# Kernel tuning notes

Hardware: AMD Instinct MI355X
Metric: run time of the kernel (lower is better)

## Reference

```python
import jax, jax.numpy as jnp
import numpy as np

N_HEADS = 16
N_KV_HEADS = 8
SOFTMAX_N = 1.0


def _apply_rope(t, cos, sin):
    # t: [B, S, H, HD]; cos/sin: [S, HD//2]
    tr = t[..., 0::2]
    ti = t[..., 1::2]
    c = cos[None, :, None, :]
    s = sin[None, :, None, :]
    out_r = tr * c - ti * s
    out_i = tr * s + ti * c
    # interleave back: (..., HD//2, 2) -> (..., HD)
    return jnp.stack([out_r, out_i], axis=-1).reshape(t.shape)


def setup_inputs() -> dict:
    key = jax.random.key(0)
    ks = jax.random.split(key, 7)
    B, S, D = 2, 2048, 2048
    HD = D // N_HEADS  # 128
    kv_dim = N_KV_HEADS * HD  # 1024
    # realistic RoPE frequencies
    theta = 10000.0
    inv_freq = 1.0 / (theta ** (np.arange(0, HD, 2, dtype=np.float32) / HD))
    angles = np.outer(np.arange(S, dtype=np.float32), inv_freq)  # [S, HD//2]
    scale = 0.02
    return {
        "x": jax.random.normal(ks[0], (B, S, D), dtype=jnp.float32),
        "freqs_cos": jnp.asarray(np.cos(angles), dtype=jnp.float32),
        "freqs_sin": jnp.asarray(np.sin(angles), dtype=jnp.float32),
        "wq": jax.random.normal(ks[1], (D, D), dtype=jnp.float32) * scale,
        "wk": jax.random.normal(ks[2], (D, kv_dim), dtype=jnp.float32) * scale,
        "wv": jax.random.normal(ks[3], (D, kv_dim), dtype=jnp.float32) * scale,
        "wo": jax.random.normal(ks[4], (D, D), dtype=jnp.float32) * scale,
    }


def reference(x, freqs_cos, freqs_sin, wq, wk, wv, wo):
    B, S, D = x.shape
    HD = D // N_HEADS
    n_rep = N_HEADS // N_KV_HEADS

    xq = (x @ wq).reshape(B, S, N_HEADS, HD)
    xk = (x @ wk).reshape(B, S, N_KV_HEADS, HD)
    xv = (x @ wv).reshape(B, S, N_KV_HEADS, HD)

    xq = _apply_rope(xq, freqs_cos, freqs_sin)
    xk = _apply_rope(xk, freqs_cos, freqs_sin)

    # repeat_kv == repeat_interleave along head dim
    xk = jnp.repeat(xk, n_rep, axis=2)
    xv = jnp.repeat(xv, n_rep, axis=2)

    q = xq.transpose(0, 2, 1, 3)  # [B,H,S,HD]
    k = xk.transpose(0, 2, 1, 3)
    v = xv.transpose(0, 2, 1, 3)

    scores = jnp.einsum('bhqd,bhkd->bhqk', q, k) / jnp.sqrt(jnp.float32(HD))
    causal = jnp.tril(jnp.ones((S, S), dtype=bool))
    scores = jnp.where(causal[None, None], scores, -jnp.inf)

    # softmax-n with shifted-zeros correction (NOT shift symmetric)
    m = jnp.max(scores, axis=-1, keepdims=True)
    e = jnp.exp(scores - m)
    denom = jnp.sum(e, axis=-1, keepdims=True) + SOFTMAX_N * jnp.exp(-m)
    attn = e / denom

    out = jnp.einsum('bhqk,bhkd->bhqd', attn, v)
    out = out.transpose(0, 2, 1, 3).reshape(B, S, D)
    return out @ wo
```

## Files before the change

### kernel.cpp

```cpp
#include <hip/hip_runtime.h>

typedef unsigned short u16;
typedef u16 u16x8 __attribute__((ext_vector_type(8)));
typedef u16 u16x4 __attribute__((ext_vector_type(4)));
typedef __bf16 bf16x8 __attribute__((ext_vector_type(8)));
typedef float f32x4 __attribute__((ext_vector_type(4)));

__device__ __forceinline__ u16 f2bf(float x) {
  unsigned u = __builtin_bit_cast(unsigned, x);
  u = (u + 0x7FFFu + ((u >> 16) & 1u)) >> 16;
  return (u16)u;
}

#define GLOAD16(gp, lp)                                                        \
  __builtin_amdgcn_global_load_lds(                                            \
      (const __attribute__((address_space(1))) unsigned int*)(gp),             \
      (__attribute__((address_space(3))) unsigned int*)(lp), 16, 0, 0)

__global__ __launch_bounds__(256) void k_cvt(const float* __restrict__ in, u16* __restrict__ out, int n4) {
  int i = blockIdx.x * 256 + threadIdx.x;
  if (i >= n4) return;
  float4 v = ((const float4*)in)[i];
  u16x4 o;
  o[0] = f2bf(v.x); o[1] = f2bf(v.y); o[2] = f2bf(v.z); o[3] = f2bf(v.w);
  ((u16x4*)out)[i] = o;
}

__global__ __launch_bounds__(256) void k_cvt_t(const float* __restrict__ in, u16* __restrict__ out, int R, int C) {
  __shared__ u16 t[64][72];
  int c0 = blockIdx.x * 64, r0 = blockIdx.y * 64;
  int tid = threadIdx.x;
  int rl = tid >> 2;
  int cl0 = (tid & 3) * 16;
#pragma unroll
  for (int j = 0; j < 4; ++j) {
    float4 v = *(const float4*)&in[(size_t)(r0 + rl) * C + c0 + cl0 + j * 4];
    t[rl][cl0 + j * 4 + 0] = f2bf(v.x);
    t[rl][cl0 + j * 4 + 1] = f2bf(v.y);
    t[rl][cl0 + j * 4 + 2] = f2bf(v.z);
    t[rl][cl0 + j * 4 + 3] = f2bf(v.w);
  }
  __syncthreads();
  int cr = tid >> 2;
  int s0 = (tid & 3) * 16;
  __align__(16) u16 tmp[16];
#pragma unroll
  for (int k = 0; k < 16; ++k) tmp[k] = t[s0 + k][cr];
  *(u16x8*)&out[(size_t)(c0 + cr) * R + r0 + s0]     = *(u16x8*)&tmp[0];
  *(u16x8*)&out[(size_t)(c0 + cr) * R + r0 + s0 + 8] = *(u16x8*)&tmp[8];
}

template <bool F32OUT>
__global__ __launch_bounds__(256) void k_gemm(const u16* __restrict__ A, const u16* __restrict__ Bt,
                                              void* __restrict__ Cout, int M, int N, int K) {
  __shared__ __align__(16) u16 lA[128 * 64];
  __shared__ __align__(16) u16 lB[128 * 64];
  int m0 = blockIdx.x * 128, n0 = blockIdx.y * 128;
  int tid = threadIdx.x;
  int wid = tid >> 6, lane = tid & 63;
  int fr = lane & 15, fg = lane >> 4;
  int wm = (wid & 1) * 64, wn = (wid >> 1) * 64;
  int srow = tid >> 3, scu = (tid & 7) * 8;
  f32x4 acc[4][4] = {};
  const int nk = K >> 6;
  for (int kt = 0; kt < nk; ++kt) {
    int k0 = kt << 6;
#pragma unroll
    for (int r = 0; r < 4; ++r) {
      int row = srow + r * 32;
      int swz = scu ^ ((row & 7) << 3);
      GLOAD16(&A[(size_t)(m0 + row) * K + k0 + swz],  &lA[row * 64 + scu]);
      GLOAD16(&Bt[(size_t)(n0 + row) * K + k0 + swz], &lB[row * 64 + scu]);
    }
    __syncthreads();
#pragma unroll
    for (int kh = 0; kh < 2; ++kh) {
      bf16x8 af[4], bf[4];
#pragma unroll
      for (int mi = 0; mi < 4; ++mi) {
        int row = wm + mi * 16 + fr;
        af[mi] = *(const bf16x8*)&lA[row * 64 + ((kh * 32 + fg * 8) ^ ((row & 7) << 3))];
      }
#pragma unroll
      for (int ni = 0; ni < 4; ++ni) {
        int row = wn + ni * 16 + fr;
        bf[ni] = *(const bf16x8*)&lB[row * 64 + ((kh * 32 + fg * 8) ^ ((row & 7) << 3))];
      }
#pragma unroll
      for (int mi = 0; mi < 4; ++mi)
#pragma unroll
        for (int ni = 0; ni < 4; ++ni)
          acc[mi][ni] = __builtin_amdgcn_mfma_f32_16x16x32_bf16(af[mi], bf[ni], acc[mi][ni], 0, 0, 0);
    }
    __syncthreads();
  }
#pragma unroll
  for (int mi = 0; mi < 4; ++mi)
#pragma unroll
    for (int ni = 0; ni < 4; ++ni)
#pragma unroll
      for (int r = 0; r < 4; ++r) {
        int row = m0 + wm + mi * 16 + fg * 4 + r;
        int col = n0 + wn + ni * 16 + fr;
        float v = acc[mi][ni][r];
        if (F32OUT) ((float*)Cout)[(size_t)row * N + col] = v;
        else        ((u16*)Cout)[(size_t)row * N + col] = f2bf(v);
      }
}

__global__ __launch_bounds__(256) void k_rope(const u16* __restrict__ qkv, const float* __restrict__ fc,
                                              const float* __restrict__ fs, u16* __restrict__ Qr,
                                              u16* __restrict__ Kr) {
  int row = blockIdx.x;
  int b = row >> 11, s = row & 2047;
  int tid = threadIdx.x;
  float4 c4 = *(const float4*)&fc[s * 64 + (tid & 15) * 4];
  float4 s4 = *(const float4*)&fs[s * 64 + (tid & 15) * 4];
  float cc[4] = {c4.x, c4.y, c4.z, c4.w};
  float ss[4] = {s4.x, s4.y, s4.z, s4.w};
  {
    bf16x8 v = *(const bf16x8*)&qkv[(size_t)row * 4096 + tid * 8];
    bf16x8 o;
    const float qs = 0.08838834764831845f;
#pragma unroll
    for (int j = 0; j < 4; ++j) {
      float e = (float)v[2 * j], od = (float)v[2 * j + 1];
      o[2 * j]     = (__bf16)((e * cc[j] - od * ss[j]) * qs);
      o[2 * j + 1] = (__bf16)((e * ss[j] + od * cc[j]) * qs);
    }
    int h = tid >> 4, d0 = (tid & 15) * 8;
    *(bf16x8*)&Qr[(((size_t)(b * 16 + h)) * 2048 + s) * 128 + d0] = o;
  }
  if (tid < 128) {
    bf16x8 v = *(const bf16x8*)&qkv[(size_t)row * 4096 + 2048 + tid * 8];
    bf16x8 o;
#pragma unroll
    for (int j = 0; j < 4; ++j) {
      float e = (float)v[2 * j], od = (float)v[2 * j + 1];
      o[2 * j]     = (__bf16)(e * cc[j] - od * ss[j]);
      o[2 * j + 1] = (__bf16)(e * ss[j] + od * cc[j]);
    }
    int hk = tid >> 4, d0 = (tid & 15) * 8;
    *(bf16x8*)&Kr[(((size_t)(b * 8 + hk)) * 2048 + s) * 128 + d0] = o;
  }
}

__global__ __launch_bounds__(256) void k_vtrans(const u16* __restrict__ qkv, u16* __restrict__ Vt) {
  __shared__ u16 t[64][72];
  int dt = blockIdx.x, st = blockIdx.y, bh = blockIdx.z;
  int b = bh >> 3, hk = bh & 7;
  int s0 = st * 64, d0 = dt * 64;
  int tid = threadIdx.x;
  int rl = tid >> 3, cs = (tid & 7) * 8;
#pragma unroll
  for (int rnd = 0; rnd < 2; ++rnd) {
    int srow = rl + rnd * 32;
    u16x8 v = *(const u16x8*)&qkv[(size_t)(b * 2048 + s0 + srow) * 4096 + 3072 + hk * 128 + d0 + cs];
#pragma unroll
    for (int k = 0; k < 8; ++k) t[srow][cs + k] = v[k];
  }
  __syncthreads();
#pragma unroll
  for (int rnd = 0; rnd < 2; ++rnd) {
    int drow = rl + rnd * 32;
    u16x8 o;
#pragma unroll
    for (int k = 0; k < 8; ++k) o[k] = t[cs + k][drow];
    *(u16x8*)&Vt[((size_t)(b * 8 + hk) * 128 + d0 + drow) * 2048 + s0 + cs] = o;
  }
}

__global__ __launch_bounds__(256) void k_attn(const u16* __restrict__ Qr, const u16* __restrict__ Kr,
                                              const u16* __restrict__ Vt, u16* __restrict__ Og) {
  const int S = 2048;
  __shared__ __align__(16) u16 lK[2][64 * 128];
  __shared__ __align__(16) u16 lV[2][128 * 64];
  __shared__ __align__(16) u16 lP[4][16 * 64];
  int h = blockIdx.y, b = blockIdx.z;
  int hk = h >> 1;
  int tid = threadIdx.x, wid = tid >> 6, lane = tid & 63;
  int fr = lane & 15, fg = lane >> 4;
  const size_t kvbase = ((size_t)(b * 8 + hk)) * S * 128;
  int ksr = tid >> 4, ksc = (tid & 15) * 8;
  int vsr = tid >> 3, vsc = (tid & 7) * 8;
  int kswz = ksc ^ ((ksr & 7) << 3);
  int vswz = vsc ^ ((vsr & 7) << 3);

#define STAGE_KV(K0, BUF)                                                                      \
  {                                                                                            \
    int k0_ = (K0);                                                                            \
    _Pragma("unroll")                                                                          \
    for (int r = 0; r < 4; ++r) {                                                              \
      GLOAD16(&Kr[kvbase + (size_t)(k0_ + ksr + r * 16) * 128 + kswz],                         \
              &lK[BUF][(ksr + r * 16) * 128 + ksc]);                                           \
      GLOAD16(&Vt[kvbase + (size_t)(vsr + r * 32) * S + k0_ + vswz],                           \
              &lV[BUF][(vsr + r * 32) * 64 + vsc]);                                            \
    }                                                                                          \
  }

  for (int pp = 0; pp < 2; ++pp) {
    int qt = pp == 0 ? (31 - (int)blockIdx.x) : (int)blockIdx.x;
    int q0 = qt * 64;
    int qw = q0 + wid * 16;
    bf16x8 qf[4];
    {
      const u16* qb = Qr + (((size_t)(b * 16 + h)) * S + qw) * 128;
#pragma unroll
      for (int ds = 0; ds < 4; ++ds)
        qf[ds] = *(const bf16x8*)&qb[fr * 128 + ds * 32 + fg * 8];
    }
    f32x4 acc[8] = {};
    float mR[4] = {-1e30f, -1e30f, -1e30f, -1e30f};
    float lRp[4] = {0.f, 0.f, 0.f, 0.f};
    int nt = qt + 1;
    STAGE_KV(0, 0);
    __syncthreads();
    int cur = 0;
    for (int t = 0; t < nt; ++t) {
      int k0 = t * 64;
      if (t + 1 < nt) STAGE_KV(k0 + 64, cur ^ 1);
      f32x4 sf[4] = {};
      __builtin_amdgcn_s_setprio(1);
#pragma unroll
      for (int kb = 0; kb < 4; ++kb)
#pragma unroll
        for (int ds = 0; ds < 4; ++ds) {
          int row = kb * 16 + fr;
          bf16x8 kf = *(const bf16x8*)&lK[cur][row * 128 + ((ds * 32 + fg * 8) ^ ((row & 7) << 3))];
          sf[kb] = __builtin_amdgcn_mfma_f32_16x16x32_bf16(qf[ds], kf, sf[kb], 0, 0, 0);
        }
      __builtin_amdgcn_s_setprio(0);
      if (k0 + 63 > qw) {
#pragma unroll
        for (int kb = 0; kb < 4; ++kb)
#pragma unroll
          for (int r = 0; r < 4; ++r)
            if (k0 + kb * 16 + fr > qw + fg * 4 + r) sf[kb][r] = -1e30f;
      }
      float pm[4];
#pragma unroll
      for (int r = 0; r < 4; ++r) {
        float v = fmaxf(fmaxf(sf[0][r], sf[1][r]), fmaxf(sf[2][r], sf[3][r]));
        v = fmaxf(v, __shfl_xor(v, 1));
        v = fmaxf(v, __shfl_xor(v, 2));
        v = fmaxf(v, __shfl_xor(v, 4));
        v = fmaxf(v, __shfl_xor(v, 8));
        pm[r] = v;
      }
      bool grow = (pm[0] > mR[0] + 8.f) | (pm[1] > mR[1] + 8.f) |
                  (pm[2] > mR[2] + 8.f) | (pm[3] > mR[3] + 8.f);
      if (__any(grow)) {
#pragma unroll
        for (int r = 0; r < 4; ++r) {
          float mn = fmaxf(mR[r], pm[r]);
          float sc = __expf(mR[r] - mn);
          mR[r] = mn;
          lRp[r] *= sc;
#pragma unroll
          for (int ni = 0; ni < 8; ++ni) acc[ni][r] *= sc;
        }
      }
#pragma unroll
      for (int kb = 0; kb < 4; ++kb)
#pragma unroll
        for (int r = 0; r < 4; ++r)
          sf[kb][r] = __expf(sf[kb][r] - mR[r]);
#pragma unroll
      for (int r = 0; r < 4; ++r)
        lRp[r] += (sf[0][r] + sf[1][r]) + (sf[2][r] + sf[3][r]);
#pragma unroll
      for (int kb = 0; kb < 4; ++kb)
#pragma unroll
        for (int r = 0; r < 4; ++r) {
          int q = fg * 4 + r;
          int cu = kb * 16 + fr;
          lP[wid][q * 64 + (cu ^ ((q & 7) << 3))] = __builtin_bit_cast(u16, (__bf16)sf[kb][r]);
        }
      __builtin_amdgcn_s_setprio(1);
#pragma unroll
      for (int kh = 0; kh < 2; ++kh) {
        bf16x8 pf = *(const bf16x8*)&lP[wid][fr * 64 + ((kh * 32 + fg * 8) ^ ((fr & 7) << 3))];
#pragma unroll
        for (int ni = 0; ni < 8; ++ni) {
          int row = ni * 16 + fr;
          bf16x8 vf = *(const bf16x8*)&lV[cur][row * 64 + ((kh * 32 + fg * 8) ^ ((row & 7) << 3))];
          acc[ni] = __builtin_amdgcn_mfma_f32_16x16x32_bf16(pf, vf, acc[ni], 0, 0, 0);
        }
      }
      __builtin_amdgcn_s_setprio(0);
      __syncthreads();
      cur ^= 1;
    }
    float rden[4];
#pragma unroll
    for (int r = 0; r < 4; ++r) {
      float s = lRp[r];
      s += __shfl_xor(s, 1);
      s += __shfl_xor(s, 2);
      s += __shfl_xor(s, 4);
      s += __shfl_xor(s, 8);
      rden[r] = 1.0f / (s + __expf(-mR[r]));
    }
#pragma unroll
    for (int ni = 0; ni < 8; ++ni)
#pragma unroll
      for (int r = 0; r < 4; ++r) {
        int q = qw + fg * 4 + r;
        int col = h * 128 + ni * 16 + fr;
        Og[((size_t)(b * S + q)) * 2048 + col] = f2bf(acc[ni][r] * rden[r]);
      }
  }
#undef STAGE_KV
}

extern "C" void kernel_launch(void* const* d_in, const int* in_sizes, int n_in,
                              void* d_out, int out_size, void* d_ws, size_t ws_size,
                              hipStream_t stream) {
  const float* x  = (const float*)d_in[0];
  const float* fc = (const float*)d_in[1];
  const float* fs = (const float*)d_in[2];
  const float* wq = (const float*)d_in[3];
  const float* wk = (const float*)d_in[4];
  const float* wv = (const float*)d_in[5];
  const float* wo = (const float*)d_in[6];

  char* p = (char*)d_ws;
  u16* xb    = (u16*)p; p += (size_t)4096 * 2048 * 2;
  u16* wqkvt = (u16*)p; p += (size_t)4096 * 2048 * 2;
  u16* wot   = (u16*)p; p += (size_t)2048 * 2048 * 2;
  u16* qkv   = (u16*)p; p += (size_t)4096 * 4096 * 2;
  u16* Qr    = (u16*)p; p += (size_t)2 * 16 * 2048 * 128 * 2;
  u16* Kr    = (u16*)p; p += (size_t)2 * 8 * 2048 * 128 * 2;
  u16* Vt    = (u16*)p; p += (size_t)2 * 8 * 2048 * 128 * 2;
  u16* Og    = xb;

  k_cvt<<<8192, 256, 0, stream>>>(x, xb, 2097152);
  k_cvt_t<<<dim3(32, 32), 256, 0, stream>>>(wq, wqkvt, 2048, 2048);
  k_cvt_t<<<dim3(16, 32), 256, 0, stream>>>(wk, wqkvt + (size_t)2048 * 2048, 2048, 1024);
  k_cvt_t<<<dim3(16, 32), 256, 0, stream>>>(wv, wqkvt + (size_t)3072 * 2048, 2048, 1024);
  k_cvt_t<<<dim3(32, 32), 256, 0, stream>>>(wo, wot, 2048, 2048);
  k_gemm<false><<<dim3(32, 32), 256, 0, stream>>>(xb, wqkvt, qkv, 4096, 4096, 2048);
  k_rope<<<4096, 256, 0, stream>>>(qkv, fc, fs, Qr, Kr);
  k_vtrans<<<dim3(2, 32, 16), 256, 0, stream>>>(qkv, Vt);
  k_attn<<<dim3(16, 16, 2), 256, 0, stream>>>(Qr, Kr, Vt, Og);
  k_gemm<true><<<dim3(32, 16), 256, 0, stream>>>(Og, wot, d_out, 4096, 2048, 2048);
}
```

Baseline: 360.9 us.

## Split attention KV loop across two wave groups with LDS softmax merge

The attention kernel now launches 512 threads per block. Two groups of four waves each process alternating KV tiles for the same query tile, and their partial max, sum and accumulators are merged through shared memory at the end. The goal is more parallelism per query tile and shorter serial KV loops. In exchange it drops the double-buffered prefetch, so every round loads then waits at a barrier with no overlap. It also adds a combine step and raises LDS use to 80 KB, which may limit occupancy.

```diff
diff --git a/kernel.cpp b/kernel.cpp
--- a/kernel.cpp
+++ b/kernel.cpp
@@ -170,38 +170,48 @@
   }
 }
 
-__global__ __launch_bounds__(256) void k_attn(const u16* __restrict__ Qr, const u16* __restrict__ Kr,
+__global__ __launch_bounds__(512) void k_attn(const u16* __restrict__ Qr, const u16* __restrict__ Kr,
                                               const u16* __restrict__ Vt, u16* __restrict__ Og) {
   const int S = 2048;
-  __shared__ __align__(16) u16 lK[2][64 * 128];
-  __shared__ __align__(16) u16 lV[2][128 * 64];
-  __shared__ __align__(16) u16 lP[4][16 * 64];
+  __shared__ __align__(16) char smem[81920];
+  u16* lK = (u16*)smem;
+  u16* lV = (u16*)(smem + 32768);
+  u16* lP = (u16*)(smem + 65536);
+  float* xm = (float*)(smem + 65536);
+  float* xl = (float*)(smem + 66048);
+  float* xacc = (float*)smem;
+
   int h = blockIdx.y, b = blockIdx.z;
   int hk = h >> 1;
   int tid = threadIdx.x, wid = tid >> 6, lane = tid & 63;
+  int grp = wid >> 2;
   int fr = lane & 15, fg = lane >> 4;
   const size_t kvbase = ((size_t)(b * 8 + hk)) * S * 128;
-  int ksr = tid >> 4, ksc = (tid & 15) * 8;
-  int vsr = tid >> 3, vsc = (tid & 7) * 8;
+  int gtid = tid & 255;
+  int ksr = gtid >> 4, ksc = (gtid & 15) * 8;
+  int vsr = gtid >> 3, vsc = (gtid & 7) * 8;
   int kswz = ksc ^ ((ksr & 7) << 3);
   int vswz = vsc ^ ((vsr & 7) << 3);
-
-#define STAGE_KV(K0, BUF)                                                                      \
+  u16* lKg = lK + grp * (64 * 128);
+  u16* lVg = lV + grp * (128 * 64);
+  u16* lPw = lP + wid * (16 * 64);
+
+#define STAGE_KV(K0)                                                                           \
   {                                                                                            \
     int k0_ = (K0);                                                                            \
     _Pragma("unroll")                                                                          \
     for (int r = 0; r < 4; ++r) {                                                              \
       GLOAD16(&Kr[kvbase + (size_t)(k0_ + ksr + r * 16) * 128 + kswz],                         \
-              &lK[BUF][(ksr + r * 16) * 128 + ksc]);                                           \
+              &lKg[(ksr + r * 16) * 128 + ksc]);                                               \
       GLOAD16(&Vt[kvbase + (size_t)(vsr + r * 32) * S + k0_ + vswz],                           \
-              &lV[BUF][(vsr + r * 32) * 64 + vsc]);                                            \
+              &lVg[(vsr + r * 32) * 64 + vsc]);                                                \
     }                                                                                          \
   }
 
   for (int pp = 0; pp < 2; ++pp) {
-    int qt = pp == 0 ? (31 - (int)blockIdx.x) : (int)blockIdx.x;
+    int qt = pp == 0 ? (15 - (int)blockIdx.x) + 16 : (int)blockIdx.x;
     int q0 = qt * 64;
-    int qw = q0 + wid * 16;
+    int qw = q0 + (wid & 3) * 16;
     bf16x8 qf[4];
     {
       const u16* qb = Qr + (((size_t)(b * 16 + h)) * S + qw) * 128;
@@ -213,85 +223,88 @@
     float mR[4] = {-1e30f, -1e30f, -1e30f, -1e30f};
     float lRp[4] = {0.f, 0.f, 0.f, 0.f};
     int nt = qt + 1;
-    STAGE_KV(0, 0);
-    __syncthreads();
-    int cur = 0;
-    for (int t = 0; t < nt; ++t) {
-      int k0 = t * 64;
-      if (t + 1 < nt) STAGE_KV(k0 + 64, cur ^ 1);
-      f32x4 sf[4] = {};
-      __builtin_amdgcn_s_setprio(1);
-#pragma unroll
-      for (int kb = 0; kb < 4; ++kb)
-#pragma unroll
-        for (int ds = 0; ds < 4; ++ds) {
-          int row = kb * 16 + fr;
-          bf16x8 kf = *(const bf16x8*)&lK[cur][row * 128 + ((ds * 32 + fg * 8) ^ ((row & 7) << 3))];
-          sf[kb] = __builtin_amdgcn_mfma_f32_16x16x32_bf16(qf[ds], kf, sf[kb], 0, 0, 0);
-        }
-      __builtin_amdgcn_s_setprio(0);
-      if (k0 + 63 > qw) {
+    int nr = (nt + 1) >> 1;
+    __syncthreads();
+    for (int rd = 0; rd < nr; ++rd) {
+      int t = 2 * rd + grp;
+      bool valid = t < nt;
+      if (valid) STAGE_KV(t * 64);
+      __syncthreads();
+      if (valid) {
+        int k0 = t * 64;
+        f32x4 sf[4] = {};
+        __builtin_amdgcn_s_setprio(1);
 #pragma unroll
         for (int kb = 0; kb < 4; ++kb)
 #pragma unroll
+          for (int ds = 0; ds < 4; ++ds) {
+            int row = kb * 16 + fr;
+            bf16x8 kf = *(const bf16x8*)&lKg[row * 128 + ((ds * 32 + fg * 8) ^ ((row & 7) << 3))];
+            sf[kb] = __builtin_amdgcn_mfma_f32_16x16x32_bf16(qf[ds], kf, sf[kb], 0, 0, 0);
+          }
+        __builtin_amdgcn_s_setprio(0);
+        if (k0 + 63 > qw) {
+#pragma unroll
+          for (int kb = 0; kb < 4; ++kb)
+#pragma unroll
+            for (int r = 0; r < 4; ++r)
+              if (k0 + kb * 16 + fr > qw + fg * 4 + r) sf[kb][r] = -1e30f;
+        }
+        float pm[4];
+#pragma unroll
+        for (int r = 0; r < 4; ++r) {
+          float v = fmaxf(fmaxf(sf[0][r], sf[1][r]), fmaxf(sf[2][r], sf[3][r]));
+          v = fmaxf(v, __shfl_xor(v, 1));
+          v = fmaxf(v, __shfl_xor(v, 2));
+          v = fmaxf(v, __shfl_xor(v, 4));
+          v = fmaxf(v, __shfl_xor(v, 8));
+          pm[r] = v;
+        }
+        bool grow = (pm[0] > mR[0] + 8.f) | (pm[1] > mR[1] + 8.f) |
+                    (pm[2] > mR[2] + 8.f) | (pm[3] > mR[3] + 8.f);
+        if (__any(grow)) {
+#pragma unroll
+          for (int r = 0; r < 4; ++r) {
+            float mn = fmaxf(mR[r], pm[r]);
+            float sc = __expf(mR[r] - mn);
+            mR[r] = mn;
+            lRp[r] *= sc;
+#pragma unroll
+            for (int ni = 0; ni < 8; ++ni) acc[ni][r] *= sc;
+          }
+        }
+#pragma unroll
+        for (int kb = 0; kb < 4; ++kb)
+#pragma unroll
           for (int r = 0; r < 4; ++r)
-            if (k0 + kb * 16 + fr > qw + fg * 4 + r) sf[kb][r] = -1e30f;
-      }
-      float pm[4];
-#pragma unroll
-      for (int r = 0; r < 4; ++r) {
-        float v = fmaxf(fmaxf(sf[0][r], sf[1][r]), fmaxf(sf[2][r], sf[3][r]));
-        v = fmaxf(v, __shfl_xor(v, 1));
-        v = fmaxf(v, __shfl_xor(v, 2));
-        v = fmaxf(v, __shfl_xor(v, 4));
-        v = fmaxf(v, __shfl_xor(v, 8));
-        pm[r] = v;
-      }
-      bool grow = (pm[0] > mR[0] + 8.f) | (pm[1] > mR[1] + 8.f) |
-                  (pm[2] > mR[2] + 8.f) | (pm[3] > mR[3] + 8.f);
-      if (__any(grow)) {
-#pragma unroll
-        for (int r = 0; r < 4; ++r) {
-          float mn = fmaxf(mR[r], pm[r]);
-          float sc = __expf(mR[r] - mn);
-          mR[r] = mn;
-          lRp[r] *= sc;
-#pragma unroll
-          for (int ni = 0; ni < 8; ++ni) acc[ni][r] *= sc;
-        }
-      }
-#pragma unroll
-      for (int kb = 0; kb < 4; ++kb)
+            sf[kb][r] = __expf(sf[kb][r] - mR[r]);
 #pragma unroll
         for (int r = 0; r < 4; ++r)
-          sf[kb][r] = __expf(sf[kb][r] - mR[r]);
-#pragma unroll
-      for (int r = 0; r < 4; ++r)
-        lRp[r] += (sf[0][r] + sf[1][r]) + (sf[2][r] + sf[3][r]);
-#pragma unroll
-      for (int kb = 0; kb < 4; ++kb)
-#pragma unroll
-        for (int r = 0; r < 4; ++r) {
-          int q = fg * 4 + r;
-          int cu = kb * 16 + fr;
-          lP[wid][q * 64 + (cu ^ ((q & 7) << 3))] = __builtin_bit_cast(u16, (__bf16)sf[kb][r]);
-        }
-      __builtin_amdgcn_s_setprio(1);
-#pragma unroll
-      for (int kh = 0; kh < 2; ++kh) {
-        bf16x8 pf = *(const bf16x8*)&lP[wid][fr * 64 + ((kh * 32 + fg * 8) ^ ((fr & 7) << 3))];
-#pragma unroll
-        for (int ni = 0; ni < 8; ++ni) {
-          int row = ni * 16 + fr;
-          bf16x8 vf = *(const bf16x8*)&lV[cur][row * 64 + ((kh * 32 + fg * 8) ^ ((row & 7) << 3))];
-          acc[ni] = __builtin_amdgcn_mfma_f32_16x16x32_bf16(pf, vf, acc[ni], 0, 0, 0);
-        }
-      }
-      __builtin_amdgcn_s_setprio(0);
+          lRp[r] += (sf[0][r] + sf[1][r]) + (sf[2][r] + sf[3][r]);
+#pragma unroll
+        for (int kb = 0; kb < 4; ++kb)
+#pragma unroll
+          for (int r = 0; r < 4; ++r) {
+            int q = fg * 4 + r;
+            int cu = kb * 16 + fr;
+            lPw[q * 64 + (cu ^ ((q & 7) << 3))] = __builtin_bit_cast(u16, (__bf16)sf[kb][r]);
+          }
+        __builtin_amdgcn_s_setprio(1);
+#pragma unroll
+        for (int kh = 0; kh < 2; ++kh) {
+          bf16x8 pf = *(const bf16x8*)&lPw[fr * 64 + ((kh * 32 + fg * 8) ^ ((fr & 7) << 3))];
+#pragma unroll
+          for (int ni = 0; ni < 8; ++ni) {
+            int row = ni * 16 + fr;
+            bf16x8 vf = *(const bf16x8*)&lVg[row * 64 + ((kh * 32 + fg * 8) ^ ((row & 7) << 3))];
+            acc[ni] = __builtin_amdgcn_mfma_f32_16x16x32_bf16(pf, vf, acc[ni], 0, 0, 0);
+          }
+        }
+        __builtin_amdgcn_s_setprio(0);
+      }
       __syncthreads();
-      cur ^= 1;
-    }
-    float rden[4];
+    }
+    float lsum[4];
 #pragma unroll
     for (int r = 0; r < 4; ++r) {
       float s = lRp[r];
@@ -299,16 +312,49 @@
       s += __shfl_xor(s, 2);
       s += __shfl_xor(s, 4);
       s += __shfl_xor(s, 8);
-      rden[r] = 1.0f / (s + __expf(-mR[r]));
-    }
-#pragma unroll
-    for (int ni = 0; ni < 8; ++ni)
+      lsum[r] = s;
+    }
+    if (fr == 0) {
 #pragma unroll
       for (int r = 0; r < 4; ++r) {
-        int q = qw + fg * 4 + r;
-        int col = h * 128 + ni * 16 + fr;
-        Og[((size_t)(b * S + q)) * 2048 + col] = f2bf(acc[ni][r] * rden[r]);
-      }
+        int row = (wid & 3) * 16 + fg * 4 + r;
+        xm[grp * 64 + row] = mR[r];
+        xl[grp * 64 + row] = lsum[r];
+      }
+    }
+    __syncthreads();
+    float eS[4], rden[4];
+#pragma unroll
+    for (int r = 0; r < 4; ++r) {
+      int row = (wid & 3) * 16 + fg * 4 + r;
+      float mA = xm[row], mB = xm[64 + row];
+      float m = fmaxf(mA, mB);
+      float eA = __expf(mA - m), eB = __expf(mB - m);
+      rden[r] = 1.0f / (xl[row] * eA + xl[64 + row] * eB + __expf(-m));
+      eS[r] = grp == 0 ? eA : eB;
+    }
+    if (grp == 0) {
+#pragma unroll
+      for (int ni = 0; ni < 8; ++ni)
+#pragma unroll
+        for (int r = 0; r < 4; ++r) {
+          int row = (wid & 3) * 16 + fg * 4 + r;
+          xacc[row * 130 + ni * 16 + fr] = acc[ni][r] * eS[r];
+        }
+    }
+    __syncthreads();
+    if (grp == 1) {
+#pragma unroll
+      for (int ni = 0; ni < 8; ++ni)
+#pragma unroll
+        for (int r = 0; r < 4; ++r) {
+          int row = (wid & 3) * 16 + fg * 4 + r;
+          float v = (acc[ni][r] * eS[r] + xacc[row * 130 + ni * 16 + fr]) * rden[r];
+          int q = qw + fg * 4 + r;
+          int col = h * 128 + ni * 16 + fr;
+          Og[((size_t)(b * S + q)) * 2048 + col] = f2bf(v);
+        }
+    }
   }
 #undef STAGE_KV
 }
@@ -342,6 +388,6 @@
   k_gemm<false><<<dim3(32, 32), 256, 0, stream>>>(xb, wqkvt, qkv, 4096, 4096, 2048);
   k_rope<<<4096, 256, 0, stream>>>(qkv, fc, fs, Qr, Kr);
   k_vtrans<<<dim3(2, 32, 16), 256, 0, stream>>>(qkv, Vt);
-  k_attn<<<dim3(16, 16, 2), 256, 0, stream>>>(Qr, Kr, Vt, Og);
+  k_attn<<<dim3(16, 16, 2), 512, 0, stream>>>(Qr, Kr, Vt, Og);
   k_gemm<true><<<dim3(32, 16), 256, 0, stream>>>(Og, wot, d_out, 4096, 2048, 2048);
 }
```

Measured after the change: 384.4 us. +6.5%, slower.

## Drop K/V double buffering and paired q-tiles; launch one block per q-tile

Applied to the files above, without the earlier changes.

The attention kernel now uses a single K/V LDS buffer, loaded synchronously at the start of each key tile, instead of prefetching the next tile into a second buffer. Each block now processes one query tile, longest first, rather than a balanced pair of tiles, so the grid doubles. This cuts LDS use per block, which may allow more resident blocks per CU, at the cost of losing load/compute overlap inside a block and the explicit load balancing from tile pairing.

```diff
diff --git a/kernel.cpp b/kernel.cpp
--- a/kernel.cpp
+++ b/kernel.cpp
@@ -173,8 +173,8 @@
 __global__ __launch_bounds__(256) void k_attn(const u16* __restrict__ Qr, const u16* __restrict__ Kr,
                                               const u16* __restrict__ Vt, u16* __restrict__ Og) {
   const int S = 2048;
-  __shared__ __align__(16) u16 lK[2][64 * 128];
-  __shared__ __align__(16) u16 lV[2][128 * 64];
+  __shared__ __align__(16) u16 lK[64 * 128];
+  __shared__ __align__(16) u16 lV[128 * 64];
   __shared__ __align__(16) u16 lP[4][16 * 64];
   int h = blockIdx.y, b = blockIdx.z;
   int hk = h >> 1;
@@ -186,131 +186,117 @@
   int kswz = ksc ^ ((ksr & 7) << 3);
   int vswz = vsc ^ ((vsr & 7) << 3);
 
-#define STAGE_KV(K0, BUF)                                                                      \
-  {                                                                                            \
-    int k0_ = (K0);                                                                            \
-    _Pragma("unroll")                                                                          \
-    for (int r = 0; r < 4; ++r) {                                                              \
-      GLOAD16(&Kr[kvbase + (size_t)(k0_ + ksr + r * 16) * 128 + kswz],                         \
-              &lK[BUF][(ksr + r * 16) * 128 + ksc]);                                           \
-      GLOAD16(&Vt[kvbase + (size_t)(vsr + r * 32) * S + k0_ + vswz],                           \
-              &lV[BUF][(vsr + r * 32) * 64 + vsc]);                                            \
-    }                                                                                          \
-  }
-
-  for (int pp = 0; pp < 2; ++pp) {
-    int qt = pp == 0 ? (31 - (int)blockIdx.x) : (int)blockIdx.x;
-    int q0 = qt * 64;
-    int qw = q0 + wid * 16;
-    bf16x8 qf[4];
-    {
-      const u16* qb = Qr + (((size_t)(b * 16 + h)) * S + qw) * 128;
-#pragma unroll
-      for (int ds = 0; ds < 4; ++ds)
-        qf[ds] = *(const bf16x8*)&qb[fr * 128 + ds * 32 + fg * 8];
-    }
-    f32x4 acc[8] = {};
-    float mR[4] = {-1e30f, -1e30f, -1e30f, -1e30f};
-    float lRp[4] = {0.f, 0.f, 0.f, 0.f};
-    int nt = qt + 1;
-    STAGE_KV(0, 0);
+  int qt = 31 - (int)blockIdx.x;
+  int q0 = qt * 64;
+  int qw = q0 + wid * 16;
+  bf16x8 qf[4];
+  {
+    const u16* qb = Qr + (((size_t)(b * 16 + h)) * S + qw) * 128;
+#pragma unroll
+    for (int ds = 0; ds < 4; ++ds)
+      qf[ds] = *(const bf16x8*)&qb[fr * 128 + ds * 32 + fg * 8];
+  }
+  f32x4 acc[8] = {};
+  float mR[4] = {-1e30f, -1e30f, -1e30f, -1e30f};
+  float lRp[4] = {0.f, 0.f, 0.f, 0.f};
+  int nt = qt + 1;
+  for (int t = 0; t < nt; ++t) {
+    int k0 = t * 64;
+#pragma unroll
+    for (int r = 0; r < 4; ++r) {
+      GLOAD16(&Kr[kvbase + (size_t)(k0 + ksr + r * 16) * 128 + kswz], &lK[(ksr + r * 16) * 128 + ksc]);
+      GLOAD16(&Vt[kvbase + (size_t)(vsr + r * 32) * S + k0 + vswz], &lV[(vsr + r * 32) * 64 + vsc]);
+    }
     __syncthreads();
-    int cur = 0;
-    for (int t = 0; t < nt; ++t) {
-      int k0 = t * 64;
-      if (t + 1 < nt) STAGE_KV(k0 + 64, cur ^ 1);
-      f32x4 sf[4] = {};
-      __builtin_amdgcn_s_setprio(1);
+    f32x4 sf[4] = {};
+    __builtin_amdgcn_s_setprio(1);
+#pragma unroll
+    for (int kb = 0; kb < 4; ++kb)
+#pragma unroll
+      for (int ds = 0; ds < 4; ++ds) {
+        int row = kb * 16 + fr;
+        bf16x8 kf = *(const bf16x8*)&lK[row * 128 + ((ds * 32 + fg * 8) ^ ((row & 7) << 3))];
+        sf[kb] = __builtin_amdgcn_mfma_f32_16x16x32_bf16(qf[ds], kf, sf[kb], 0, 0, 0);
+      }
+    __builtin_amdgcn_s_setprio(0);
+    if (k0 + 63 > qw) {
 #pragma unroll
       for (int kb = 0; kb < 4; ++kb)
 #pragma unroll
-        for (int ds = 0; ds < 4; ++ds) {
-          int row = kb * 16 + fr;
-          bf16x8 kf = *(const bf16x8*)&lK[cur][row * 128 + ((ds * 32 + fg * 8) ^ ((row & 7) << 3))];
-          sf[kb] = __builtin_amdgcn_mfma_f32_16x16x32_bf16(qf[ds], kf, sf[kb], 0, 0, 0);
-        }
-      __builtin_amdgcn_s_setprio(0);
-      if (k0 + 63 > qw) {
-#pragma unroll
-        for (int kb = 0; kb < 4; ++kb)
-#pragma unroll
-          for (int r = 0; r < 4; ++r)
-            if (k0 + kb * 16 + fr > qw + fg * 4 + r) sf[kb][r] = -1e30f;
-      }
-      float pm[4];
+        for (int r = 0; r < 4; ++r)
+          if (k0 + kb * 16 + fr > qw + fg * 4 + r) sf[kb][r] = -1e30f;
+    }
+    float pm[4];
+#pragma unroll
+    for (int r = 0; r < 4; ++r) {
+      float v = fmaxf(fmaxf(sf[0][r], sf[1][r]), fmaxf(sf[2][r], sf[3][r]));
+      v = fmaxf(v, __shfl_xor(v, 1));
+      v = fmaxf(v, __shfl_xor(v, 2));
+      v = fmaxf(v, __shfl_xor(v, 4));
+      v = fmaxf(v, __shfl_xor(v, 8));
+      pm[r] = v;
+    }
+    bool grow = (pm[0] > mR[0] + 8.f) | (pm[1] > mR[1] + 8.f) |
+                (pm[2] > mR[2] + 8.f) | (pm[3] > mR[3] + 8.f);
+    if (__any(grow)) {
 #pragma unroll
       for (int r = 0; r < 4; ++r) {
-        float v = fmaxf(fmaxf(sf[0][r], sf[1][r]), fmaxf(sf[2][r], sf[3][r]));
-        v = fmaxf(v, __shfl_xor(v, 1));
-        v = fmaxf(v, __shfl_xor(v, 2));
-        v = fmaxf(v, __shfl_xor(v, 4));
-        v = fmaxf(v, __shfl_xor(v, 8));
-        pm[r] = v;
-      }
-      bool grow = (pm[0] > mR[0] + 8.f) | (pm[1] > mR[1] + 8.f) |
-                  (pm[2] > mR[2] + 8.f) | (pm[3] > mR[3] + 8.f);
-      if (__any(grow)) {
-#pragma unroll
-        for (int r = 0; r < 4; ++r) {
-          float mn = fmaxf(mR[r], pm[r]);
-          float sc = __expf(mR[r] - mn);
-          mR[r] = mn;
-          lRp[r] *= sc;
-#pragma unroll
-          for (int ni = 0; ni < 8; ++ni) acc[ni][r] *= sc;
-        }
-      }
-#pragma unroll
-      for (int kb = 0; kb < 4; ++kb)
-#pragma unroll
-        for (int r = 0; r < 4; ++r)
-          sf[kb][r] = __expf(sf[kb][r] - mR[r]);
+        float mn = fmaxf(mR[r], pm[r]);
+        float sc = __expf(mR[r] - mn);
+        mR[r] = mn;
+        lRp[r] *= sc;
+#pragma unroll
+        for (int ni = 0; ni < 8; ++ni) acc[ni][r] *= sc;
+      }
+    }
+#pragma unroll
+    for (int kb = 0; kb < 4; ++kb)
 #pragma unroll
       for (int r = 0; r < 4; ++r)
-        lRp[r] += (sf[0][r] + sf[1][r]) + (sf[2][r] + sf[3][r]);
-#pragma unroll
-      for (int kb = 0; kb < 4; ++kb)
-#pragma unroll
-        for (int r = 0; r < 4; ++r) {
-          int q = fg * 4 + r;
-          int cu = kb * 16 + fr;
-          lP[wid][q * 64 + (cu ^ ((q & 7) << 3))] = __builtin_bit_cast(u16, (__bf16)sf[kb][r]);
-        }
-      __builtin_amdgcn_s_setprio(1);
-#pragma unroll
-      for (int kh = 0; kh < 2; ++kh) {
-        bf16x8 pf = *(const bf16x8*)&lP[wid][fr * 64 + ((kh * 32 + fg * 8) ^ ((fr & 7) << 3))];
-#pragma unroll
-        for (int ni = 0; ni < 8; ++ni) {
-          int row = ni * 16 + fr;
-          bf16x8 vf = *(const bf16x8*)&lV[cur][row * 64 + ((kh * 32 + fg * 8) ^ ((row & 7) << 3))];
-          acc[ni] = __builtin_amdgcn_mfma_f32_16x16x32_bf16(pf, vf, acc[ni], 0, 0, 0);
-        }
-      }
-      __builtin_amdgcn_s_setprio(0);
-      __syncthreads();
-      cur ^= 1;
-    }
-    float rden[4];
+        sf[kb][r] = __expf(sf[kb][r] - mR[r]);
+#pragma unroll
+    for (int r = 0; r < 4; ++r)
+      lRp[r] += (sf[0][r] + sf[1][r]) + (sf[2][r] + sf[3][r]);
+#pragma unroll
+    for (int kb = 0; kb < 4; ++kb)
+#pragma unroll
+      for (int r = 0; r < 4; ++r) {
+        int q = fg * 4 + r;
+        int cu = kb * 16 + fr;
+        lP[wid][q * 64 + (cu ^ ((q & 7) << 3))] = __builtin_bit_cast(u16, (__bf16)sf[kb][r]);
+      }
+    __builtin_amdgcn_s_setprio(1);
+#pragma unroll
+    for (int kh = 0; kh < 2; ++kh) {
+      bf16x8 pf = *(const bf16x8*)&lP[wid][fr * 64 + ((kh * 32 + fg * 8) ^ ((fr & 7) << 3))];
+#pragma unroll
+      for (int ni = 0; ni < 8; ++ni) {
+        int row = ni * 16 + fr;
+        bf16x8 vf = *(const bf16x8*)&lV[row * 64 + ((kh * 32 + fg * 8) ^ ((row & 7) << 3))];
+        acc[ni] = __builtin_amdgcn_mfma_f32_16x16x32_bf16(pf, vf, acc[ni], 0, 0, 0);
+      }
+    }
+    __builtin_amdgcn_s_setprio(0);
+    __syncthreads();
+  }
+  float rden[4];
+#pragma unroll
+  for (int r = 0; r < 4; ++r) {
+    float s = lRp[r];
+    s += __shfl_xor(s, 1);
+    s += __shfl_xor(s, 2);
+    s += __shfl_xor(s, 4);
+    s += __shfl_xor(s, 8);
+    rden[r] = 1.0f / (s + __expf(-mR[r]));
+  }
+#pragma unroll
+  for (int ni = 0; ni < 8; ++ni)
 #pragma unroll
     for (int r = 0; r < 4; ++r) {
-      float s = lRp[r];
-      s += __shfl_xor(s, 1);
-      s += __shfl_xor(s, 2);
-      s += __shfl_xor(s, 4);
-      s += __shfl_xor(s, 8);
-      rden[r] = 1.0f / (s + __expf(-mR[r]));
-    }
-#pragma unroll
-    for (int ni = 0; ni < 8; ++ni)
-#pragma unroll
-      for (int r = 0; r < 4; ++r) {
-        int q = qw + fg * 4 + r;
-        int col = h * 128 + ni * 16 + fr;
-        Og[((size_t)(b * S + q)) * 2048 + col] = f2bf(acc[ni][r] * rden[r]);
-      }
-  }
-#undef STAGE_KV
+      int q = qw + fg * 4 + r;
+      int col = h * 128 + ni * 16 + fr;
+      Og[((size_t)(b * S + q)) * 2048 + col] = f2bf(acc[ni][r] * rden[r]);
+    }
 }
 
 extern "C" void kernel_launch(void* const* d_in, const int* in_sizes, int n_in,
@@ -342,6 +328,6 @@
   k_gemm<false><<<dim3(32, 32), 256, 0, stream>>>(xb, wqkvt, qkv, 4096, 4096, 2048);
   k_rope<<<4096, 256, 0, stream>>>(qkv, fc, fs, Qr, Kr);
   k_vtrans<<<dim3(2, 32, 16), 256, 0, stream>>>(qkv, Vt);
-  k_attn<<<dim3(16, 16, 2), 256, 0, stream>>>(Qr, Kr, Vt, Og);
+  k_attn<<<dim3(32, 16, 2), 256, 0, stream>>>(Qr, Kr, Vt, Og);
   k_gemm<true><<<dim3(32, 16), 256, 0, stream>>>(Og, wot, d_out, 4096, 2048, 2048);
 }
```

New measurement: 429.6 us. 19.0% more time.
